# Optimization experiments

Hardware: AMD Instinct MI355X
Metric: run time of the kernel (lower is better)

## Reference

```python
import jax, jax.numpy as jnp
import numpy as np

B, T, I, H = 64, 512, 512, 1024


def setup_inputs() -> dict:
    key = jax.random.key(0)
    ks = jax.random.split(key, 14)
    s = 0.05
    d = {"x": jax.random.normal(ks[0], (B, T, I), dtype=jnp.float32)}
    names = ["W_i", "W_f", "W_c", "W_o"]
    for n, k in zip(names, ks[1:5]):
        d[n] = jax.random.normal(k, (H, I), dtype=jnp.float32) * s
    for n, k in zip(["U_i", "U_f", "U_c", "U_o"], ks[5:9]):
        d[n] = jax.random.normal(k, (H, H), dtype=jnp.float32) * s
    for n, k in zip(["b_i", "b_f", "b_c", "b_o"], ks[9:13]):
        d[n] = jax.random.normal(k, (H,), dtype=jnp.float32) * s
    return d


def _lstm(x, W_i, W_f, W_c, W_o, b_i, b_f, b_c, b_o, U_i, U_f, U_c, U_o):
    # Precompute all input-gate preactivations in big GEMMs: (B,T,H)
    xi = jnp.einsum("bti,hi->bth", x, W_i) + b_i
    xf = jnp.einsum("bti,hi->bth", x, W_f) + b_f
    xg = jnp.einsum("bti,hi->bth", x, W_c) + b_c
    xo = jnp.einsum("bti,hi->bth", x, W_o) + b_o
    # time-major for scan: (T,B,H)
    xs = (xi.transpose(1, 0, 2), xf.transpose(1, 0, 2),
          xg.transpose(1, 0, 2), xo.transpose(1, 0, 2))
    h0 = jnp.zeros((x.shape[0], U_i.shape[0]), dtype=x.dtype)
    c0 = jnp.zeros_like(h0)

    def step(carry, xt):
        h, c = carry
        xi_t, xf_t, xg_t, xo_t = xt
        i = jax.nn.sigmoid(xi_t + h @ U_i.T)
        f = jax.nn.sigmoid(xf_t + h @ U_f.T)
        g = jnp.tanh(xg_t + h @ U_c.T)
        o = jax.nn.sigmoid(xo_t + h @ U_o.T)
        c_n = f * c + i * g
        h_n = o * jnp.tanh(c_n)
        return (h_n, c_n), h_n

    (h_n, c_n), ys = jax.lax.scan(step, (h0, c0), xs)
    out = ys.transpose(1, 0, 2)  # (B,T,H), batch_first
    return out, h_n, c_n


def reference(x, W_i, W_f, W_c, W_o, U_i, U_f, U_c, U_o, b_i, b_f, b_c, b_o):
    return _lstm(x, W_i, W_f, W_c, W_o, b_i, b_f, b_c, b_o, U_i, U_f, U_c, U_o)
```

## Files before the change

### kernel.cpp

```cpp
#include <hip/hip_runtime.h>
#include <hip/hip_bf16.h>


typedef __attribute__((ext_vector_type(8))) short bf16x8;
typedef __attribute__((ext_vector_type(4))) float f32x4;
typedef unsigned int uint32;
typedef unsigned long long u64;

static __device__ __forceinline__ unsigned short f2bf(float f) {
    union { float f; unsigned int u; } v; v.f = f;
    unsigned int r = v.u + 0x7fffu + ((v.u >> 16) & 1u);
    return (unsigned short)(r >> 16);
}

#define NB   64
#define NT   512
#define NI   512
#define NH   1024
#define NWG  64


__global__ void prep3(const float* __restrict__ x,
                      const float* __restrict__ Wi, const float* __restrict__ Wf,
                      const float* __restrict__ Wc, const float* __restrict__ Wo,
                      unsigned short* __restrict__ Wb, unsigned short* __restrict__ xTb,
                      int* __restrict__ flags)
{
    const int NW = 4 * NH * NI;
    const int NX = NB * NT * NI;
    const int NF = NT * 1024;
    const int total = NW + NX + NF;
    for (int idx = blockIdx.x * blockDim.x + threadIdx.x; idx < total;
         idx += gridDim.x * blockDim.x) {
        if (idx < NW) {
            int g = idx >> 19;
            int off = idx & 524287;
            const float* W = (g == 0) ? Wi : (g == 1) ? Wf : (g == 2) ? Wc : Wo;
            Wb[idx] = f2bf(W[off]);
        } else if (idx < NW + NX) {
            int e = idx - NW;
            int b = e >> 18;
            int r = e & 262143;
            int t = r >> 9;
            int i = r & 511;
            xTb[((size_t)t * NB + b) * NI + i] = f2bf(x[e]);
        } else {
            flags[idx - NW - NX] = 0;
        }
    }
}

__global__ __launch_bounds__(1024) void lstm_persist3(
    const float* __restrict__ Ui, const float* __restrict__ Uf,
    const float* __restrict__ Uc, const float* __restrict__ Uo,
    const float* __restrict__ b_i, const float* __restrict__ b_f,
    const float* __restrict__ b_c, const float* __restrict__ b_o,
    const unsigned short* __restrict__ Wb, const unsigned short* __restrict__ xT,
    unsigned short* __restrict__ hb,
    int* __restrict__ flags,
    float* __restrict__ out, float* __restrict__ hn_arr, float* __restrict__ cn_arr)
{
    __shared__ __align__(16) unsigned char smem[163840];
    unsigned char* Us   = smem;
    unsigned char* stg0 = smem + 131072;
    unsigned char* stg1 = smem + 147456;
    float* gacc = (float*)(smem + 131072);

    const int tid  = threadIdx.x;
    const int lane = tid & 63;
    const int wv   = tid >> 6;
    const int g    = wv & 3;
    const int mt   = wv >> 2;
    const int rm   = lane & 15;
    const int kg   = (lane >> 4) * 8;
    const int wg   = blockIdx.x;
    const int u0   = wg * 16;

    for (int i = 0; i < 8; ++i) {
        int unit = i * 1024 + tid;
        int row  = unit >> 7;
        int k0   = (unit & 127) * 8;
        int gg   = row >> 4;
        const float* src = (gg == 0 ? Ui : gg == 1 ? Uf : gg == 2 ? Uc : Uo)
                           + (size_t)(u0 + (row & 15)) * NH + k0;
        bf16x8 v;
        #pragma unroll
        for (int j = 0; j < 8; ++j) v[j] = (short)f2bf(src[j]);
        *(bf16x8*)(Us + row * 2048 + ((k0 * 2) ^ ((row & 15) << 4))) = v;
    }

    const int bl = tid >> 4, ul = tid & 15;
    const float rbi = b_i[u0 + ul], rbf = b_f[u0 + ul];
    const float rbc = b_c[u0 + ul], rbo = b_o[u0 + ul];
    float creg = 0.f;

    const int sb   = bl;
    const int k8   = ul * 8;
    const int soff = sb * 256 + ((k8 * 2) ^ ((sb & 15) << 4));

    const int abase = (mt * 16 + rm) * 256;
    const int ubase = (g * 16 + rm) * 2048;
    const size_t wrow = ((size_t)(g * NH + u0 + rm)) * NI;

    __syncthreads();

    for (int t = 0; t < NT; ++t) {
        f32x4 acc = {0.f, 0.f, 0.f, 0.f};

        const unsigned short* xrow = xT + ((size_t)t * NB + sb) * NI;
        uint4 xr[4];
        #pragma unroll
        for (int c = 0; c < 4; ++c)
            xr[c] = *(const uint4*)(xrow + c * 128 + k8);
        *(uint4*)(stg0 + soff) = xr[0];
        __syncthreads();
        #pragma unroll
        for (int c = 0; c < 4; ++c) {
            const unsigned char* sbuf = (c & 1) ? stg1 : stg0;
            #pragma unroll
            for (int kk = 0; kk < 4; ++kk) {
                const int kloc = kk * 32 + kg;
                bf16x8 af = *(const bf16x8*)(sbuf + abase + ((kloc * 2) ^ (rm << 4)));
                bf16x8 bw = *(const bf16x8*)(Wb + wrow + c * 128 + kloc);
                acc = __builtin_amdgcn_mfma_f32_16x16x32_bf16(af, bw, acc, 0, 0, 0);
            }
            if (c < 3) {
                unsigned char* dbuf = ((c + 1) & 1) ? stg1 : stg0;
                *(uint4*)(dbuf + soff) = xr[c + 1];
            }
            __syncthreads();
        }

        if (t > 0) {
            if (wv == 0) {
                const int* fp = flags + (size_t)(t - 1) * 1024 + lane * 16;
                int spins = 0;
                while (__hip_atomic_load(fp, __ATOMIC_RELAXED,
                                         __HIP_MEMORY_SCOPE_AGENT) == 0 &&
                       spins < (1 << 20)) {
                    __builtin_amdgcn_s_sleep(2);
                    ++spins;
                }
            }
            __syncthreads();

            const u64* hsrc = (const u64*)hb + (size_t)((t - 1) % 3) * 16384
                              + (size_t)sb * 256 + (size_t)ul * 2;
            u64 hr[8][2];
            #pragma unroll
            for (int c = 0; c < 8; ++c) {
                hr[c][0] = __hip_atomic_load(hsrc + c * 32, __ATOMIC_RELAXED,
                                             __HIP_MEMORY_SCOPE_AGENT);
                hr[c][1] = __hip_atomic_load(hsrc + c * 32 + 1, __ATOMIC_RELAXED,
                                             __HIP_MEMORY_SCOPE_AGENT);
            }
            {
                uint4 v; v.x = (uint32)hr[0][0]; v.y = (uint32)(hr[0][0] >> 32);
                v.z = (uint32)hr[0][1]; v.w = (uint32)(hr[0][1] >> 32);
                *(uint4*)(stg0 + soff) = v;
            }
            __syncthreads();
            #pragma unroll
            for (int c = 0; c < 8; ++c) {
                const unsigned char* sbuf = (c & 1) ? stg1 : stg0;
                #pragma unroll
                for (int kk = 0; kk < 4; ++kk) {
                    const int kloc = kk * 32 + kg;
                    bf16x8 af = *(const bf16x8*)(sbuf + abase + ((kloc * 2) ^ (rm << 4)));
                    const int kglob = c * 128 + kloc;
                    bf16x8 bu = *(const bf16x8*)(Us + ubase + ((kglob * 2) ^ (rm << 4)));
                    acc = __builtin_amdgcn_mfma_f32_16x16x32_bf16(af, bu, acc, 0, 0, 0);
                }
                if (c < 7) {
                    unsigned char* dbuf = ((c + 1) & 1) ? stg1 : stg0;
                    uint4 v; v.x = (uint32)hr[c + 1][0]; v.y = (uint32)(hr[c + 1][0] >> 32);
                    v.z = (uint32)hr[c + 1][1]; v.w = (uint32)(hr[c + 1][1] >> 32);
                    *(uint4*)(dbuf + soff) = v;
                }
                __syncthreads();
            }
        }

        #pragma unroll
        for (int r = 0; r < 4; ++r) {
            const int brow = mt * 16 + (lane >> 4) * 4 + r;
            gacc[(g * 64 + brow) * 16 + rm] = acc[r];
        }
        __syncthreads();

        {
            float pi = gacc[(0 * 64 + bl) * 16 + ul] + rbi;
            float pf = gacc[(1 * 64 + bl) * 16 + ul] + rbf;
            float pg = gacc[(2 * 64 + bl) * 16 + ul] + rbc;
            float po = gacc[(3 * 64 + bl) * 16 + ul] + rbo;
            float ig  = 1.f / (1.f + __expf(-pi));
            float fg  = 1.f / (1.f + __expf(-pf));
            float gg2 = tanhf(pg);
            float og  = 1.f / (1.f + __expf(-po));
            float cn2 = fg * creg + ig * gg2;
            float hn2 = og * tanhf(cn2);
            creg = cn2;
            out[((size_t)bl * NT + t) * NH + u0 + ul] = hn2;

            unsigned short h16 = f2bf(hn2);
            uint32 lo = (uint32)h16 |
                        ((((uint32)__shfl_down((int)h16, 1, 64)) & 0xffffu) << 16);
            u64 p4 = (u64)lo | ((u64)(uint32)__shfl_down((int)lo, 2, 64) << 32);
            if ((ul & 3) == 0) {
                u64* hd = (u64*)hb + (size_t)(t % 3) * 16384
                          + (size_t)bl * 256 + (size_t)((u0 + ul) >> 2);
                __hip_atomic_store(hd, p4, __ATOMIC_RELAXED,
                                   __HIP_MEMORY_SCOPE_AGENT);
            }
            if (t == NT - 1) {
                hn_arr[(size_t)bl * NH + u0 + ul] = hn2;
                cn_arr[(size_t)bl * NH + u0 + ul] = cn2;
            }
        }

        __syncthreads();
        if (tid == 0)
            __hip_atomic_store(flags + (size_t)t * 1024 + wg * 16, 1,
                               __ATOMIC_RELAXED, __HIP_MEMORY_SCOPE_AGENT);
    }
}


__global__ void lstm_prep(const float* __restrict__ Ui, const float* __restrict__ Uf,
                          const float* __restrict__ Uc, const float* __restrict__ Uo,
                          const float* __restrict__ Wi, const float* __restrict__ Wf,
                          const float* __restrict__ Wc, const float* __restrict__ Wo,
                          unsigned short* __restrict__ Ub, unsigned short* __restrict__ Wb,
                          unsigned short* __restrict__ hb0, float* __restrict__ c_state)
{
    const int NU = 4 * NH * NH;
    const int NW = 4 * NH * NI;
    const int NS = NB * NH;
    const int total = NU + NW + NS + NS;
    for (int idx = blockIdx.x * blockDim.x + threadIdx.x; idx < total;
         idx += gridDim.x * blockDim.x) {
        if (idx < NU) {
            int g = idx >> 20;
            int off = idx & (NH * NH - 1);
            const float* U = (g == 0) ? Ui : (g == 1) ? Uf : (g == 2) ? Uc : Uo;
            Ub[idx] = f2bf(U[off]);
        } else if (idx < NU + NW) {
            int j = idx - NU;
            int g = j >> 19;
            int off = j & (NH * NI - 1);
            const float* W = (g == 0) ? Wi : (g == 1) ? Wf : (g == 2) ? Wc : Wo;
            Wb[j] = f2bf(W[off]);
        } else if (idx < NU + NW + NS) {
            hb0[idx - NU - NW] = 0;
        } else {
            c_state[idx - NU - NW - NS] = 0.0f;
        }
    }
}

__global__ __launch_bounds__(256) void lstm_step(
    const float* __restrict__ x,
    const unsigned short* __restrict__ Ub,
    const unsigned short* __restrict__ Wb,
    const unsigned short* __restrict__ hb_in,
    unsigned short* __restrict__ hb_out,
    const float* __restrict__ bi, const float* __restrict__ bff,
    const float* __restrict__ bc, const float* __restrict__ bo,
    float* __restrict__ out, float* __restrict__ c_state,
    float* __restrict__ hn_out, int t)
{
    __shared__ float gacc[4][32][16];
    const int lane = threadIdx.x & 63;
    const int g    = threadIdx.x >> 6;
    const int u0   = (blockIdx.x >> 1) * 16;
    const int b0   = (blockIdx.x & 1) * 32;
    const int rm   = lane & 15;
    const int kg   = (lane >> 4) * 8;

    f32x4 acc0 = {0.f, 0.f, 0.f, 0.f};
    f32x4 acc1 = {0.f, 0.f, 0.f, 0.f};

    const unsigned short* Ug  = Ub + (size_t)g * (NH * NH) + (size_t)(u0 + rm) * NH;
    const unsigned short* h0p = hb_in + (size_t)(b0 + rm) * NH;
    const unsigned short* h1p = hb_in + (size_t)(b0 + 16 + rm) * NH;
    #pragma unroll 4
    for (int k0 = 0; k0 < NH; k0 += 32) {
        bf16x8 bfrag = *(const bf16x8*)(Ug + k0 + kg);
        bf16x8 a0 = *(const bf16x8*)(h0p + k0 + kg);
        bf16x8 a1 = *(const bf16x8*)(h1p + k0 + kg);
        acc0 = __builtin_amdgcn_mfma_f32_16x16x32_bf16(a0, bfrag, acc0, 0, 0, 0);
        acc1 = __builtin_amdgcn_mfma_f32_16x16x32_bf16(a1, bfrag, acc1, 0, 0, 0);
    }
    const unsigned short* Wg  = Wb + (size_t)g * (NH * NI) + (size_t)(u0 + rm) * NI;
    const float* x0p = x + ((size_t)(b0 + rm) * NT + t) * NI;
    const float* x1p = x + ((size_t)(b0 + 16 + rm) * NT + t) * NI;
    #pragma unroll 2
    for (int k0 = 0; k0 < NI; k0 += 32) {
        bf16x8 bfrag = *(const bf16x8*)(Wg + k0 + kg);
        f32x4 lo0 = *(const f32x4*)(x0p + k0 + kg);
        f32x4 hi0 = *(const f32x4*)(x0p + k0 + kg + 4);
        f32x4 lo1 = *(const f32x4*)(x1p + k0 + kg);
        f32x4 hi1 = *(const f32x4*)(x1p + k0 + kg + 4);
        bf16x8 a0, a1;
        #pragma unroll
        for (int j = 0; j < 4; j++) {
            a0[j]     = (short)f2bf(lo0[j]);
            a0[j + 4] = (short)f2bf(hi0[j]);
            a1[j]     = (short)f2bf(lo1[j]);
            a1[j + 4] = (short)f2bf(hi1[j]);
        }
        acc0 = __builtin_amdgcn_mfma_f32_16x16x32_bf16(a0, bfrag, acc0, 0, 0, 0);
        acc1 = __builtin_amdgcn_mfma_f32_16x16x32_bf16(a1, bfrag, acc1, 0, 0, 0);
    }
    const int row4 = (lane >> 4) * 4;
    #pragma unroll
    for (int r = 0; r < 4; r++) {
        gacc[g][row4 + r][rm]      = acc0[r];
        gacc[g][16 + row4 + r][rm] = acc1[r];
    }
    __syncthreads();
    for (int p = threadIdx.x; p < 512; p += 256) {
        int bl = p >> 4, ul = p & 15;
        int b = b0 + bl, u = u0 + ul;
        float pi = gacc[0][bl][ul] + bi[u];
        float pf = gacc[1][bl][ul] + bff[u];
        float pg = gacc[2][bl][ul] + bc[u];
        float po = gacc[3][bl][ul] + bo[u];
        float ig = 1.f / (1.f + __expf(-pi));
        float fg = 1.f / (1.f + __expf(-pf));
        float gg = tanhf(pg);
        float og = 1.f / (1.f + __expf(-po));
        float cold = c_state[(size_t)b * NH + u];
        float cn = fg * cold + ig * gg;
        float hn = og * tanhf(cn);
        c_state[(size_t)b * NH + u] = cn;
        out[((size_t)b * NT + t) * NH + u] = hn;
        hb_out[(size_t)b * NH + u] = f2bf(hn);
        if (hn_out) hn_out[(size_t)b * NH + u] = hn;
    }
}


extern "C" void kernel_launch(void* const* d_in, const int* in_sizes, int n_in,
                              void* d_out, int out_size, void* d_ws, size_t ws_size,
                              hipStream_t stream) {
    const float* x  = (const float*)d_in[0];
    const float* Wi = (const float*)d_in[1];
    const float* Wf = (const float*)d_in[2];
    const float* Wc = (const float*)d_in[3];
    const float* Wo = (const float*)d_in[4];
    const float* Ui = (const float*)d_in[5];
    const float* Uf = (const float*)d_in[6];
    const float* Uc = (const float*)d_in[7];
    const float* Uo = (const float*)d_in[8];
    const float* bi = (const float*)d_in[9];
    const float* bf = (const float*)d_in[10];
    const float* bc = (const float*)d_in[11];
    const float* bo = (const float*)d_in[12];

    float* out = (float*)d_out;
    float* hn  = out + (size_t)NB * NT * NH;
    float* cn  = hn + (size_t)NB * NH;

    const size_t NEED3 = 40239104ULL;
    if (ws_size >= NEED3) {
        char* ws = (char*)d_ws;
        unsigned short* Wb = (unsigned short*)ws;
        unsigned short* xT = (unsigned short*)(ws + 4194304);
        unsigned short* hb = (unsigned short*)(ws + 37748736);
        int* flags         = (int*)(ws + 38141952);
        prep3<<<2048, 256, 0, stream>>>(x, Wi, Wf, Wc, Wo, Wb, xT, flags);
        lstm_persist3<<<NWG, 1024, 0, stream>>>(Ui, Uf, Uc, Uo, bi, bf, bc, bo,
                                                Wb, xT, hb, flags, out, hn, cn);
    } else {
        char* ws = (char*)d_ws;
        unsigned short* Ub  = (unsigned short*)ws;
        unsigned short* Wb  = (unsigned short*)(ws + 8388608);
        unsigned short* hb0 = (unsigned short*)(ws + 12582912);
        unsigned short* hb1 = (unsigned short*)(ws + 12713984);
        float* c_state = cn;
        lstm_prep<<<1024, 256, 0, stream>>>(Ui, Uf, Uc, Uo, Wi, Wf, Wc, Wo,
                                            Ub, Wb, hb0, c_state);
        for (int t = 0; t < NT; t++) {
            unsigned short* hin  = (t & 1) ? hb1 : hb0;
            unsigned short* hout = (t & 1) ? hb0 : hb1;
            lstm_step<<<128, 256, 0, stream>>>(
                x, Ub, Wb, hin, hout, bi, bf, bc, bo,
                out, c_state, (t == NT - 1) ? hn : (float*)nullptr, t);
        }
    }
}
```

Baseline: 6.838 ms.

## Load MFMA A-operands directly from global memory, removing LDS staging and barriers

```diff
diff --git a/kernel.cpp b/kernel.cpp
--- a/kernel.cpp
+++ b/kernel.cpp
@@ -4,6 +4,7 @@
 
 typedef __attribute__((ext_vector_type(8))) short bf16x8;
 typedef __attribute__((ext_vector_type(4))) float f32x4;
+typedef __attribute__((ext_vector_type(4))) unsigned int u32x4;
 typedef unsigned int uint32;
 typedef unsigned long long u64;
 
@@ -50,7 +51,31 @@
     }
 }
 
-__global__ __launch_bounds__(1024) void lstm_persist3(
+#define HLOAD4(V0, V1, V2, V3, O0, O1, O2, O3)                                  \
+    asm volatile("global_load_dwordx4 %0, %4, off offset:" O0 " sc1\n\t"        \
+                 "global_load_dwordx4 %1, %4, off offset:" O1 " sc1\n\t"        \
+                 "global_load_dwordx4 %2, %4, off offset:" O2 " sc1\n\t"        \
+                 "global_load_dwordx4 %3, %4, off offset:" O3 " sc1"            \
+                 : "=v"(V0), "=v"(V1), "=v"(V2), "=v"(V3)                       \
+                 : "v"(hP) : "memory")
+
+#define VMWAIT(N)                                                               \
+    do { asm volatile("s_waitcnt vmcnt(" #N ")" ::: "memory");                  \
+         __builtin_amdgcn_sched_barrier(0); } while (0)
+
+#define HMFMA4(ACC, V0, V1, V2, V3, KB)                                         \
+    do {                                                                        \
+        bf16x8 u_0 = *(const bf16x8*)(Us + ubase + ((((KB) + 0   + kg) * 2) ^ (rm << 4))); \
+        ACC = __builtin_amdgcn_mfma_f32_16x16x32_bf16(__builtin_bit_cast(bf16x8, V0), u_0, ACC, 0, 0, 0); \
+        bf16x8 u_1 = *(const bf16x8*)(Us + ubase + ((((KB) + 32  + kg) * 2) ^ (rm << 4))); \
+        ACC = __builtin_amdgcn_mfma_f32_16x16x32_bf16(__builtin_bit_cast(bf16x8, V1), u_1, ACC, 0, 0, 0); \
+        bf16x8 u_2 = *(const bf16x8*)(Us + ubase + ((((KB) + 64  + kg) * 2) ^ (rm << 4))); \
+        ACC = __builtin_amdgcn_mfma_f32_16x16x32_bf16(__builtin_bit_cast(bf16x8, V2), u_2, ACC, 0, 0, 0); \
+        bf16x8 u_3 = *(const bf16x8*)(Us + ubase + ((((KB) + 96  + kg) * 2) ^ (rm << 4))); \
+        ACC = __builtin_amdgcn_mfma_f32_16x16x32_bf16(__builtin_bit_cast(bf16x8, V3), u_3, ACC, 0, 0, 0); \
+    } while (0)
+
+__global__ __launch_bounds__(1024) void lstm_persist4(
     const float* __restrict__ Ui, const float* __restrict__ Uf,
     const float* __restrict__ Uc, const float* __restrict__ Uo,
     const float* __restrict__ b_i, const float* __restrict__ b_f,
@@ -60,10 +85,8 @@
     int* __restrict__ flags,
     float* __restrict__ out, float* __restrict__ hn_arr, float* __restrict__ cn_arr)
 {
-    __shared__ __align__(16) unsigned char smem[163840];
-    unsigned char* Us   = smem;
-    unsigned char* stg0 = smem + 131072;
-    unsigned char* stg1 = smem + 147456;
+    __shared__ __align__(16) unsigned char smem[147456];
+    unsigned char* Us = smem;
     float* gacc = (float*)(smem + 131072);
 
     const int tid  = threadIdx.x;
@@ -94,41 +117,28 @@
     const float rbc = b_c[u0 + ul], rbo = b_o[u0 + ul];
     float creg = 0.f;
 
-    const int sb   = bl;
-    const int k8   = ul * 8;
-    const int soff = sb * 256 + ((k8 * 2) ^ ((sb & 15) << 4));
-
-    const int abase = (mt * 16 + rm) * 256;
     const int ubase = (g * 16 + rm) * 2048;
     const size_t wrow = ((size_t)(g * NH + u0 + rm)) * NI;
+    const unsigned short* wp = Wb + wrow + kg;
 
     __syncthreads();
 
     for (int t = 0; t < NT; ++t) {
-        f32x4 acc = {0.f, 0.f, 0.f, 0.f};
-
-        const unsigned short* xrow = xT + ((size_t)t * NB + sb) * NI;
-        uint4 xr[4];
-        #pragma unroll
-        for (int c = 0; c < 4; ++c)
-            xr[c] = *(const uint4*)(xrow + c * 128 + k8);
-        *(uint4*)(stg0 + soff) = xr[0];
-        __syncthreads();
-        #pragma unroll
-        for (int c = 0; c < 4; ++c) {
-            const unsigned char* sbuf = (c & 1) ? stg1 : stg0;
+        f32x4 accx = {0.f, 0.f, 0.f, 0.f};
+        f32x4 acc0 = {0.f, 0.f, 0.f, 0.f};
+        f32x4 acc1 = {0.f, 0.f, 0.f, 0.f};
+
+        {
+            const unsigned short* xp = xT + ((size_t)t * NB + mt * 16 + rm) * NI + kg;
             #pragma unroll
-            for (int kk = 0; kk < 4; ++kk) {
-                const int kloc = kk * 32 + kg;
-                bf16x8 af = *(const bf16x8*)(sbuf + abase + ((kloc * 2) ^ (rm << 4)));
-                bf16x8 bw = *(const bf16x8*)(Wb + wrow + c * 128 + kloc);
-                acc = __builtin_amdgcn_mfma_f32_16x16x32_bf16(af, bw, acc, 0, 0, 0);
+            for (int c = 0; c < 4; ++c) {
+                #pragma unroll
+                for (int kk = 0; kk < 4; ++kk) {
+                    bf16x8 ax = *(const bf16x8*)(xp + c * 128 + kk * 32);
+                    bf16x8 bw = *(const bf16x8*)(wp + c * 128 + kk * 32);
+                    accx = __builtin_amdgcn_mfma_f32_16x16x32_bf16(ax, bw, accx, 0, 0, 0);
+                }
             }
-            if (c < 3) {
-                unsigned char* dbuf = ((c + 1) & 1) ? stg1 : stg0;
-                *(uint4*)(dbuf + soff) = xr[c + 1];
-            }
-            __syncthreads();
         }
 
         if (t > 0) {
@@ -137,57 +147,43 @@
                 int spins = 0;
                 while (__hip_atomic_load(fp, __ATOMIC_RELAXED,
                                          __HIP_MEMORY_SCOPE_AGENT) == 0 &&
-                       spins < (1 << 20)) {
-                    __builtin_amdgcn_s_sleep(2);
+                       spins < (1 << 16)) {
+                    __builtin_amdgcn_s_sleep(1);
                     ++spins;
                 }
             }
             __syncthreads();
 
-            const u64* hsrc = (const u64*)hb + (size_t)((t - 1) % 3) * 16384
-                              + (size_t)sb * 256 + (size_t)ul * 2;
-            u64 hr[8][2];
-            #pragma unroll
-            for (int c = 0; c < 8; ++c) {
-                hr[c][0] = __hip_atomic_load(hsrc + c * 32, __ATOMIC_RELAXED,
-                                             __HIP_MEMORY_SCOPE_AGENT);
-                hr[c][1] = __hip_atomic_load(hsrc + c * 32 + 1, __ATOMIC_RELAXED,
-                                             __HIP_MEMORY_SCOPE_AGENT);
-            }
-            {
-                uint4 v; v.x = (uint32)hr[0][0]; v.y = (uint32)(hr[0][0] >> 32);
-                v.z = (uint32)hr[0][1]; v.w = (uint32)(hr[0][1] >> 32);
-                *(uint4*)(stg0 + soff) = v;
-            }
-            __syncthreads();
-            #pragma unroll
-            for (int c = 0; c < 8; ++c) {
-                const unsigned char* sbuf = (c & 1) ? stg1 : stg0;
-                #pragma unroll
-                for (int kk = 0; kk < 4; ++kk) {
-                    const int kloc = kk * 32 + kg;
-                    bf16x8 af = *(const bf16x8*)(sbuf + abase + ((kloc * 2) ^ (rm << 4)));
-                    const int kglob = c * 128 + kloc;
-                    bf16x8 bu = *(const bf16x8*)(Us + ubase + ((kglob * 2) ^ (rm << 4)));
-                    acc = __builtin_amdgcn_mfma_f32_16x16x32_bf16(af, bu, acc, 0, 0, 0);
-                }
-                if (c < 7) {
-                    unsigned char* dbuf = ((c + 1) & 1) ? stg1 : stg0;
-                    uint4 v; v.x = (uint32)hr[c + 1][0]; v.y = (uint32)(hr[c + 1][0] >> 32);
-                    v.z = (uint32)hr[c + 1][1]; v.w = (uint32)(hr[c + 1][1] >> 32);
-                    *(uint4*)(dbuf + soff) = v;
-                }
-                __syncthreads();
-            }
+            const char* hP = (const char*)hb + ((size_t)((t - 1) % 3) << 17)
+                             + ((size_t)(mt * 16 + rm) << 11) + (kg << 1);
+            u32x4 fa0, fa1, fa2, fa3, fb0, fb1, fb2, fb3;
+            u32x4 fc0, fc1, fc2, fc3, fd0, fd1, fd2, fd3;
+            HLOAD4(fa0, fa1, fa2, fa3, "0",   "64",  "128", "192");
+            HLOAD4(fb0, fb1, fb2, fb3, "256", "320", "384", "448");
+            HLOAD4(fc0, fc1, fc2, fc3, "512", "576", "640", "704");
+            HLOAD4(fd0, fd1, fd2, fd3, "768", "832", "896", "960");
+            VMWAIT(12); HMFMA4(acc0, fa0, fa1, fa2, fa3, 0);
+            HLOAD4(fa0, fa1, fa2, fa3, "1024", "1088", "1152", "1216");
+            VMWAIT(12); HMFMA4(acc1, fb0, fb1, fb2, fb3, 128);
+            HLOAD4(fb0, fb1, fb2, fb3, "1280", "1344", "1408", "1472");
+            VMWAIT(12); HMFMA4(acc0, fc0, fc1, fc2, fc3, 256);
+            HLOAD4(fc0, fc1, fc2, fc3, "1536", "1600", "1664", "1728");
+            VMWAIT(12); HMFMA4(acc1, fd0, fd1, fd2, fd3, 384);
+            HLOAD4(fd0, fd1, fd2, fd3, "1792", "1856", "1920", "1984");
+            VMWAIT(12); HMFMA4(acc0, fa0, fa1, fa2, fa3, 512);
+            VMWAIT(8);  HMFMA4(acc1, fb0, fb1, fb2, fb3, 640);
+            VMWAIT(4);  HMFMA4(acc0, fc0, fc1, fc2, fc3, 768);
+            VMWAIT(0);  HMFMA4(acc1, fd0, fd1, fd2, fd3, 896);
         }
 
         #pragma unroll
         for (int r = 0; r < 4; ++r) {
             const int brow = mt * 16 + (lane >> 4) * 4 + r;
-            gacc[(g * 64 + brow) * 16 + rm] = acc[r];
+            gacc[(g * 64 + brow) * 16 + rm] = accx[r] + acc0[r] + acc1[r];
         }
         __syncthreads();
 
+        float hn2, cn2;
         {
             float pi = gacc[(0 * 64 + bl) * 16 + ul] + rbi;
             float pf = gacc[(1 * 64 + bl) * 16 + ul] + rbf;
@@ -197,10 +193,9 @@
             float fg  = 1.f / (1.f + __expf(-pf));
             float gg2 = tanhf(pg);
             float og  = 1.f / (1.f + __expf(-po));
-            float cn2 = fg * creg + ig * gg2;
-            float hn2 = og * tanhf(cn2);
+            cn2 = fg * creg + ig * gg2;
+            hn2 = og * tanhf(cn2);
             creg = cn2;
-            out[((size_t)bl * NT + t) * NH + u0 + ul] = hn2;
 
             unsigned short h16 = f2bf(hn2);
             uint32 lo = (uint32)h16 |
@@ -212,16 +207,18 @@
                 __hip_atomic_store(hd, p4, __ATOMIC_RELAXED,
                                    __HIP_MEMORY_SCOPE_AGENT);
             }
-            if (t == NT - 1) {
-                hn_arr[(size_t)bl * NH + u0 + ul] = hn2;
-                cn_arr[(size_t)bl * NH + u0 + ul] = cn2;
-            }
         }
 
         __syncthreads();
         if (tid == 0)
             __hip_atomic_store(flags + (size_t)t * 1024 + wg * 16, 1,
                                __ATOMIC_RELAXED, __HIP_MEMORY_SCOPE_AGENT);
+
+        out[((size_t)bl * NT + t) * NH + u0 + ul] = hn2;
+        if (t == NT - 1) {
+            hn_arr[(size_t)bl * NH + u0 + ul] = hn2;
+            cn_arr[(size_t)bl * NH + u0 + ul] = cn2;
+        }
     }
 }
 
@@ -370,7 +367,7 @@
         unsigned short* hb = (unsigned short*)(ws + 37748736);
         int* flags         = (int*)(ws + 38141952);
         prep3<<<2048, 256, 0, stream>>>(x, Wi, Wf, Wc, Wo, Wb, xT, flags);
-        lstm_persist3<<<NWG, 1024, 0, stream>>>(Ui, Uf, Uc, Uo, bi, bf, bc, bo,
+        lstm_persist4<<<NWG, 1024, 0, stream>>>(Ui, Uf, Uc, Uo, bi, bf, bc, bo,
                                                 Wb, xT, hb, flags, out, hn, cn);
     } else {
         char* ws = (char*)d_ws;
```

New measurement: 15.12 ms. 121% more time.

## Pipeline recurrent h loads with vmcnt waits and split accumulators in persistent LSTM

Applied to the files above, without the earlier changes.

```diff
diff --git a/kernel.cpp b/kernel.cpp
--- a/kernel.cpp
+++ b/kernel.cpp
@@ -4,6 +4,7 @@
 
 typedef __attribute__((ext_vector_type(8))) short bf16x8;
 typedef __attribute__((ext_vector_type(4))) float f32x4;
+typedef __attribute__((ext_vector_type(4))) unsigned int u32x4;
 typedef unsigned int uint32;
 typedef unsigned long long u64;
 
@@ -50,7 +51,24 @@
     }
 }
 
-__global__ __launch_bounds__(1024) void lstm_persist3(
+#define VMWAIT(N)                                                               \
+    do { asm volatile("s_waitcnt vmcnt(" #N ")" ::: "memory");                  \
+         __builtin_amdgcn_sched_barrier(0); } while (0)
+
+static __device__ __forceinline__ void chunk_mfma_u(
+    f32x4& acc, const unsigned char* sbuf, const unsigned char* Us,
+    int abase, int ubase, int kb, int kg, int rm)
+{
+    #pragma unroll
+    for (int kk = 0; kk < 4; ++kk) {
+        const int kloc = kk * 32 + kg;
+        bf16x8 af = *(const bf16x8*)(sbuf + abase + ((kloc * 2) ^ (rm << 4)));
+        bf16x8 bu = *(const bf16x8*)(Us + ubase + (((kb + kloc) * 2) ^ (rm << 4)));
+        acc = __builtin_amdgcn_mfma_f32_16x16x32_bf16(af, bu, acc, 0, 0, 0);
+    }
+}
+
+__global__ __launch_bounds__(1024) void lstm_persist6(
     const float* __restrict__ Ui, const float* __restrict__ Uf,
     const float* __restrict__ Uc, const float* __restrict__ Uo,
     const float* __restrict__ b_i, const float* __restrict__ b_f,
@@ -101,34 +119,34 @@
     const int abase = (mt * 16 + rm) * 256;
     const int ubase = (g * 16 + rm) * 2048;
     const size_t wrow = ((size_t)(g * NH + u0 + rm)) * NI;
+    const unsigned short* wp = Wb + wrow + kg;
 
     __syncthreads();
 
     for (int t = 0; t < NT; ++t) {
-        f32x4 acc = {0.f, 0.f, 0.f, 0.f};
-
-        const unsigned short* xrow = xT + ((size_t)t * NB + sb) * NI;
-        uint4 xr[4];
-        #pragma unroll
-        for (int c = 0; c < 4; ++c)
-            xr[c] = *(const uint4*)(xrow + c * 128 + k8);
-        *(uint4*)(stg0 + soff) = xr[0];
-        __syncthreads();
-        #pragma unroll
-        for (int c = 0; c < 4; ++c) {
-            const unsigned char* sbuf = (c & 1) ? stg1 : stg0;
+        f32x4 accx = {0.f, 0.f, 0.f, 0.f};
+        f32x4 acc0 = {0.f, 0.f, 0.f, 0.f};
+        f32x4 acc1 = {0.f, 0.f, 0.f, 0.f};
+
+        {
+            const unsigned short* xrow = xT + ((size_t)t * NB + sb) * NI;
+            uint4 xr[4];
             #pragma unroll
-            for (int kk = 0; kk < 4; ++kk) {
-                const int kloc = kk * 32 + kg;
-                bf16x8 af = *(const bf16x8*)(sbuf + abase + ((kloc * 2) ^ (rm << 4)));
-                bf16x8 bw = *(const bf16x8*)(Wb + wrow + c * 128 + kloc);
-                acc = __builtin_amdgcn_mfma_f32_16x16x32_bf16(af, bw, acc, 0, 0, 0);
+            for (int c = 0; c < 4; ++c)
+                xr[c] = *(const uint4*)(xrow + c * 128 + k8);
+            #pragma unroll
+            for (int c = 0; c < 4; ++c) {
+                unsigned char* dbuf = (c & 1) ? stg1 : stg0;
+                *(uint4*)(dbuf + soff) = xr[c];
+                __syncthreads();
+                #pragma unroll
+                for (int kk = 0; kk < 4; ++kk) {
+                    const int kloc = kk * 32 + kg;
+                    bf16x8 af = *(const bf16x8*)(dbuf + abase + ((kloc * 2) ^ (rm << 4)));
+                    bf16x8 bw = *(const bf16x8*)(wp + c * 128 + kk * 32);
+                    accx = __builtin_amdgcn_mfma_f32_16x16x32_bf16(af, bw, accx, 0, 0, 0);
+                }
             }
-            if (c < 3) {
-                unsigned char* dbuf = ((c + 1) & 1) ? stg1 : stg0;
-                *(uint4*)(dbuf + soff) = xr[c + 1];
-            }
-            __syncthreads();
         }
 
         if (t > 0) {
@@ -137,57 +155,59 @@
                 int spins = 0;
                 while (__hip_atomic_load(fp, __ATOMIC_RELAXED,
                                          __HIP_MEMORY_SCOPE_AGENT) == 0 &&
-                       spins < (1 << 20)) {
-                    __builtin_amdgcn_s_sleep(2);
+                       spins < (1 << 16)) {
+                    __builtin_amdgcn_s_sleep(1);
                     ++spins;
                 }
             }
             __syncthreads();
 
-            const u64* hsrc = (const u64*)hb + (size_t)((t - 1) % 3) * 16384
-                              + (size_t)sb * 256 + (size_t)ul * 2;
-            u64 hr[8][2];
-            #pragma unroll
-            for (int c = 0; c < 8; ++c) {
-                hr[c][0] = __hip_atomic_load(hsrc + c * 32, __ATOMIC_RELAXED,
-                                             __HIP_MEMORY_SCOPE_AGENT);
-                hr[c][1] = __hip_atomic_load(hsrc + c * 32 + 1, __ATOMIC_RELAXED,
-                                             __HIP_MEMORY_SCOPE_AGENT);
-            }
-            {
-                uint4 v; v.x = (uint32)hr[0][0]; v.y = (uint32)(hr[0][0] >> 32);
-                v.z = (uint32)hr[0][1]; v.w = (uint32)(hr[0][1] >> 32);
-                *(uint4*)(stg0 + soff) = v;
-            }
-            __syncthreads();
-            #pragma unroll
-            for (int c = 0; c < 8; ++c) {
-                const unsigned char* sbuf = (c & 1) ? stg1 : stg0;
-                #pragma unroll
-                for (int kk = 0; kk < 4; ++kk) {
-                    const int kloc = kk * 32 + kg;
-                    bf16x8 af = *(const bf16x8*)(sbuf + abase + ((kloc * 2) ^ (rm << 4)));
-                    const int kglob = c * 128 + kloc;
-                    bf16x8 bu = *(const bf16x8*)(Us + ubase + ((kglob * 2) ^ (rm << 4)));
-                    acc = __builtin_amdgcn_mfma_f32_16x16x32_bf16(af, bu, acc, 0, 0, 0);
-                }
-                if (c < 7) {
-                    unsigned char* dbuf = ((c + 1) & 1) ? stg1 : stg0;
-                    uint4 v; v.x = (uint32)hr[c + 1][0]; v.y = (uint32)(hr[c + 1][0] >> 32);
-                    v.z = (uint32)hr[c + 1][1]; v.w = (uint32)(hr[c + 1][1] >> 32);
-                    *(uint4*)(dbuf + soff) = v;
-                }
-                __syncthreads();
-            }
+            const char* hP = (const char*)hb + ((size_t)((t - 1) % 3) << 17)
+                             + ((size_t)sb << 11) + ((size_t)ul << 4);
+            u32x4 h0, h1, h2, h3, h4, h5, h6, h7;
+            asm volatile(
+                "global_load_dwordx4 %0, %8, off offset:0    sc1\n\t"
+                "global_load_dwordx4 %1, %8, off offset:256  sc1\n\t"
+                "global_load_dwordx4 %2, %8, off offset:512  sc1\n\t"
+                "global_load_dwordx4 %3, %8, off offset:768  sc1\n\t"
+                "global_load_dwordx4 %4, %8, off offset:1024 sc1\n\t"
+                "global_load_dwordx4 %5, %8, off offset:1280 sc1\n\t"
+                "global_load_dwordx4 %6, %8, off offset:1536 sc1\n\t"
+                "global_load_dwordx4 %7, %8, off offset:1792 sc1"
+                : "=v"(h0), "=v"(h1), "=v"(h2), "=v"(h3),
+                  "=v"(h4), "=v"(h5), "=v"(h6), "=v"(h7)
+                : "v"(hP) : "memory");
+
+            #define HSTEP(C, HV, WN, ACC)                                        \
+                do {                                                              \
+                    VMWAIT(WN);                                                   \
+                    unsigned char* dbuf_ = ((C) & 1) ? stg1 : stg0;               \
+                    *(u32x4*)(dbuf_ + soff) = HV;                                 \
+                    asm volatile("s_waitcnt lgkmcnt(0)" ::: "memory");            \
+                    __builtin_amdgcn_s_barrier();                                 \
+                    __builtin_amdgcn_sched_barrier(0);                            \
+                    chunk_mfma_u(ACC, dbuf_, Us, abase, ubase, (C) * 128, kg, rm);\
+                } while (0)
+
+            HSTEP(0, h0, 7, acc0);
+            HSTEP(1, h1, 6, acc1);
+            HSTEP(2, h2, 5, acc0);
+            HSTEP(3, h3, 4, acc1);
+            HSTEP(4, h4, 3, acc0);
+            HSTEP(5, h5, 2, acc1);
+            HSTEP(6, h6, 1, acc0);
+            HSTEP(7, h7, 0, acc1);
+            #undef HSTEP
         }
 
         #pragma unroll
         for (int r = 0; r < 4; ++r) {
             const int brow = mt * 16 + (lane >> 4) * 4 + r;
-            gacc[(g * 64 + brow) * 16 + rm] = acc[r];
+            gacc[(g * 64 + brow) * 16 + rm] = accx[r] + acc0[r] + acc1[r];
         }
         __syncthreads();
 
+        float hn2, cn2;
         {
             float pi = gacc[(0 * 64 + bl) * 16 + ul] + rbi;
             float pf = gacc[(1 * 64 + bl) * 16 + ul] + rbf;
@@ -197,10 +217,9 @@
             float fg  = 1.f / (1.f + __expf(-pf));
             float gg2 = tanhf(pg);
             float og  = 1.f / (1.f + __expf(-po));
-            float cn2 = fg * creg + ig * gg2;
-            float hn2 = og * tanhf(cn2);
+            cn2 = fg * creg + ig * gg2;
+            hn2 = og * tanhf(cn2);
             creg = cn2;
-            out[((size_t)bl * NT + t) * NH + u0 + ul] = hn2;
 
             unsigned short h16 = f2bf(hn2);
             uint32 lo = (uint32)h16 |
@@ -212,16 +231,18 @@
                 __hip_atomic_store(hd, p4, __ATOMIC_RELAXED,
                                    __HIP_MEMORY_SCOPE_AGENT);
             }
-            if (t == NT - 1) {
-                hn_arr[(size_t)bl * NH + u0 + ul] = hn2;
-                cn_arr[(size_t)bl * NH + u0 + ul] = cn2;
-            }
         }
 
         __syncthreads();
         if (tid == 0)
             __hip_atomic_store(flags + (size_t)t * 1024 + wg * 16, 1,
                                __ATOMIC_RELAXED, __HIP_MEMORY_SCOPE_AGENT);
+
+        out[((size_t)bl * NT + t) * NH + u0 + ul] = hn2;
+        if (t == NT - 1) {
+            hn_arr[(size_t)bl * NH + u0 + ul] = hn2;
+            cn_arr[(size_t)bl * NH + u0 + ul] = cn2;
+        }
     }
 }
 
@@ -370,7 +391,7 @@
         unsigned short* hb = (unsigned short*)(ws + 37748736);
         int* flags         = (int*)(ws + 38141952);
         prep3<<<2048, 256, 0, stream>>>(x, Wi, Wf, Wc, Wo, Wb, xT, flags);
-        lstm_persist3<<<NWG, 1024, 0, stream>>>(Ui, Uf, Uc, Uo, bi, bf, bc, bo,
+        lstm_persist6<<<NWG, 1024, 0, stream>>>(Ui, Uf, Uc, Uo, bi, bf, bc, bo,
                                                 Wb, xT, hb, flags, out, hn, cn);
     } else {
         char* ws = (char*)d_ws;
```

New measurement: 7.111 ms. 1.04x slower.
